# Performance work log

Measured on AMD Instinct MI355X. Metric: run time of the kernel, lower is better.

## Reference

```python
import jax, jax.numpy as jnp
import numpy as np

ALPHA = 0.2  # LeakyReLU negative slope
NEG_BIG = -9e15

def setup_inputs() -> dict:
    key = jax.random.key(0)
    k1, k2, k3, k4 = jax.random.split(key, 4)
    N, F_in, F_out = 8192, 512, 64
    inp = jax.random.normal(k1, (N, F_in), dtype=jnp.float32)
    adj = jax.random.randint(k2, (N, N), 0, 2, dtype=jnp.int32)
    W = jax.random.normal(k3, (F_in, F_out), dtype=jnp.float32) * (1.414 / np.sqrt(F_in + F_out))
    a = jax.random.normal(k4, (2 * F_out, 1), dtype=jnp.float32) * 0.1
    return {"input": inp, "adj": adj, "W": W, "a": a}

def reference(input, adj, W, a):
    # h: [N, F_out]
    h = input @ W
    F_out = h.shape[1]
    # Decompose a into a1 (source part) and a2 (target part):
    a1 = a[:F_out, 0]   # [F_out]
    a2 = a[F_out:, 0]   # [F_out]
    s1 = h @ a1         # [N]
    s2 = h @ a2         # [N]
    e = s1[:, None] + s2[None, :]                      # [N, N]
    e = jnp.where(e > 0, e, ALPHA * e)                 # LeakyReLU
    e = jnp.where(adj > 0, e, jnp.float32(NEG_BIG))    # mask non-edges
    attention = jax.nn.softmax(e, axis=1)              # [N, N]
    # dropout with p=0.0 / eval mode -> identity
    h_prime = attention @ h                            # [N, F_out]
    return h_prime
```

## Files before the change

### kernel.cpp

```cpp
#include <hip/hip_runtime.h>
#include <hip/hip_bf16.h>

constexpr int N    = 8192;
constexpr int FIN  = 512;
constexpr int FOUT = 64;
constexpr int NSPLIT = 8;
constexpr int JCHUNK = N / NSPLIT;
constexpr int NSLICE = 4;
constexpr int JS     = JCHUNK / NSLICE;
constexpr int LROW   = JS + 8;

typedef __attribute__((ext_vector_type(8))) short short8;
typedef __attribute__((ext_vector_type(4))) float f32x4;

union BF2U { unsigned int u; __hip_bfloat162 h; };

__global__ __launch_bounds__(256) void k1_proj(
    const float* __restrict__ input, const float* __restrict__ W,
    const float* __restrict__ a, __hip_bfloat16* __restrict__ hbT,
    float* __restrict__ E1, float* __restrict__ F1,
    float* __restrict__ E2, float* __restrict__ F2)
{
    __shared__ __hip_bfloat16 tile[8][64];
    const int tid  = threadIdx.x;
    const int col  = tid & 63;
    const int g    = tid >> 6;
    const int rbase = blockIdx.x * 8;

    float acc[2] = {0.f, 0.f};
    const float* in0 = input + (size_t)(rbase + g * 2) * FIN;

    for (int k = 0; k < FIN; k += 8) {
        float w[8];
        #pragma unroll
        for (int q = 0; q < 8; ++q) w[q] = W[(k + q) * FOUT + col];
        const float4 x0a = *(const float4*)(in0 + 0 * FIN + k);
        const float4 x0b = *(const float4*)(in0 + 0 * FIN + k + 4);
        const float4 x1a = *(const float4*)(in0 + 1 * FIN + k);
        const float4 x1b = *(const float4*)(in0 + 1 * FIN + k + 4);
        acc[0] = fmaf(x0a.w, w[3], fmaf(x0a.z, w[2], fmaf(x0a.y, w[1], fmaf(x0a.x, w[0], acc[0]))));
        acc[0] = fmaf(x0b.w, w[7], fmaf(x0b.z, w[6], fmaf(x0b.y, w[5], fmaf(x0b.x, w[4], acc[0]))));
        acc[1] = fmaf(x1a.w, w[3], fmaf(x1a.z, w[2], fmaf(x1a.y, w[1], fmaf(x1a.x, w[0], acc[1]))));
        acc[1] = fmaf(x1b.w, w[7], fmaf(x1b.z, w[6], fmaf(x1b.y, w[5], fmaf(x1b.x, w[4], acc[1]))));
    }

    const float a1c = a[col];
    const float a2c = a[FOUT + col];
    #pragma unroll
    for (int q = 0; q < 2; ++q) {
        float r1 = acc[q] * a1c;
        float r2 = acc[q] * a2c;
        #pragma unroll
        for (int off = 32; off >= 1; off >>= 1) {
            r1 += __shfl_xor(r1, off, 64);
            r2 += __shfl_xor(r2, off, 64);
        }
        if (col == 0) {
            const int i = rbase + g * 2 + q;
            E1[i] = __expf(r1);
            F1[i] = __expf(0.2f * r1);
            E2[i] = __expf(r2);
            F2[i] = __expf(0.2f * r2);
        }
        tile[g * 2 + q][col] = __float2bfloat16(acc[q]);
    }
    __syncthreads();

    if (tid < 128) {
        const int c = tid >> 1, part = tid & 1;
        unsigned short v[4];
        #pragma unroll
        for (int u = 0; u < 4; ++u) {
            __hip_bfloat16 hv = tile[part * 4 + u][c];
            v[u] = *reinterpret_cast<unsigned short*>(&hv);
        }
        *(ushort4*)((unsigned short*)hbT + (size_t)c * N + rbase + part * 4) =
            make_ushort4(v[0], v[1], v[2], v[3]);
    }
}

__global__ __launch_bounds__(256, 4) void k2_attn(
    const int* __restrict__ adj,
    const float* __restrict__ E1, const float* __restrict__ F1,
    const float* __restrict__ E2, const float* __restrict__ F2,
    const unsigned short* __restrict__ hbT,
    float* __restrict__ pAcc, float* __restrict__ pZ)
{
    __shared__ unsigned short Bl[64 * LROW];
    __shared__ unsigned int   Ml[64 * 9];
    __shared__ float          E2l[JS];
    __shared__ float          F2l[JS];

    const int r   = blockIdx.x;
    const int s   = blockIdx.y;
    const int tid = threadIdx.x;
    const int w     = tid >> 6;
    const int lane  = tid & 63;
    const int row16 = lane & 15;
    const int quad  = lane >> 4;

    const int iloc = w * 16 + row16;
    const int i    = r * 64 + iloc;
    const float E1i = E1[i];
    const float F1i = F1[i];

    short8 ones;
    #pragma unroll
    for (int q = 0; q < 8; ++q) ones[q] = (short)0x3F80;

    f32x4 acc0 = {0.f, 0.f, 0.f, 0.f};
    f32x4 acc1 = {0.f, 0.f, 0.f, 0.f};
    f32x4 acc2 = {0.f, 0.f, 0.f, 0.f};
    f32x4 acc3 = {0.f, 0.f, 0.f, 0.f};
    f32x4 accz = {0.f, 0.f, 0.f, 0.f};

    for (int sl = 0; sl < NSLICE; ++sl) {
        const int jbeg = s * JCHUNK + sl * JS;

        #pragma unroll
        for (int rr = 0; rr < 8; ++rr) {
            const int seg = rr * 256 + tid;
            const int f = seg >> 5, o = seg & 31;
            const short8 v = *(const short8*)((const short*)hbT + (size_t)f * N + jbeg + o * 8);
            *(short8*)(&Bl[f * LROW + o * 8]) = v;
        }
        {
            unsigned char* Mlb = (unsigned char*)Ml;
            #pragma unroll
            for (int it = 0; it < 16; ++it) {
                const int rloc = it * 4 + w;
                const int4 av = *(const int4*)(adj + (size_t)(r * 64 + rloc) * N + jbeg + lane * 4);
                unsigned int nib =
                    (av.x != 0 ? 1u : 0u) | (av.y != 0 ? 2u : 0u) |
                    (av.z != 0 ? 4u : 0u) | (av.w != 0 ? 8u : 0u);
                const unsigned int other = __shfl_xor(nib, 1, 64);
                if (!(lane & 1))
                    Mlb[rloc * 36 + (lane >> 1)] = (unsigned char)(nib | (other << 4));
            }
        }
        E2l[tid] = E2[jbeg + tid];
        F2l[tid] = F2[jbeg + tid];
        __syncthreads();

        #pragma unroll
        for (int it = 0; it < JS / 32; ++it) {
            const int jj = it * 32 + quad * 8;

            const unsigned int mword = Ml[iloc * 9 + it];
            const unsigned int mbyte = (mword >> (8 * quad)) & 0xffu;

            const float4 eA = *(const float4*)(&E2l[jj]);
            const float4 eB = *(const float4*)(&E2l[jj + 4]);
            const float4 fA = *(const float4*)(&F2l[jj]);
            const float4 fB = *(const float4*)(&F2l[jj + 4]);

            const short8 b0 = *(const short8*)(&Bl[(row16 +  0) * LROW + jj]);
            const short8 b1 = *(const short8*)(&Bl[(row16 + 16) * LROW + jj]);
            const short8 b2 = *(const short8*)(&Bl[(row16 + 32) * LROW + jj]);
            const short8 b3 = *(const short8*)(&Bl[(row16 + 48) * LROW + jj]);

            float e2v[8], f2v[8];
            e2v[0] = eA.x; e2v[1] = eA.y; e2v[2] = eA.z; e2v[3] = eA.w;
            e2v[4] = eB.x; e2v[5] = eB.y; e2v[6] = eB.z; e2v[7] = eB.w;
            f2v[0] = fA.x; f2v[1] = fA.y; f2v[2] = fA.z; f2v[3] = fA.w;
            f2v[4] = fB.x; f2v[5] = fB.y; f2v[6] = fB.z; f2v[7] = fB.w;

            float pv[8];
            #pragma unroll
            for (int j = 0; j < 8; ++j) {
                float p = fmaxf(E1i * e2v[j], F1i * f2v[j]);
                pv[j] = ((mbyte >> j) & 1u) ? p : 0.f;
            }

            short8 afrag;
            #pragma unroll
            for (int jp = 0; jp < 4; ++jp) {
                BF2U cv;
                cv.h = __float22bfloat162_rn(make_float2(pv[2 * jp], pv[2 * jp + 1]));
                afrag[2 * jp]     = (short)(cv.u & 0xffffu);
                afrag[2 * jp + 1] = (short)(cv.u >> 16);
            }

            acc0 = __builtin_amdgcn_mfma_f32_16x16x32_bf16(afrag, b0, acc0, 0, 0, 0);
            acc1 = __builtin_amdgcn_mfma_f32_16x16x32_bf16(afrag, b1, acc1, 0, 0, 0);
            acc2 = __builtin_amdgcn_mfma_f32_16x16x32_bf16(afrag, b2, acc2, 0, 0, 0);
            acc3 = __builtin_amdgcn_mfma_f32_16x16x32_bf16(afrag, b3, acc3, 0, 0, 0);
            accz = __builtin_amdgcn_mfma_f32_16x16x32_bf16(afrag, ones, accz, 0, 0, 0);
        }
        __syncthreads();
    }

    if (row16 == 0) {
        #pragma unroll
        for (int reg = 0; reg < 4; ++reg)
            pZ[(size_t)s * N + r * 64 + w * 16 + quad * 4 + reg] = accz[reg];
    }

    float* outp = pAcc + ((size_t)s * N + (size_t)r * 64 + w * 16) * FOUT;
    #pragma unroll
    for (int reg = 0; reg < 4; ++reg) {
        const int row = quad * 4 + reg;
        outp[row * FOUT + ( 0 + row16)] = acc0[reg];
        outp[row * FOUT + (16 + row16)] = acc1[reg];
        outp[row * FOUT + (32 + row16)] = acc2[reg];
        outp[row * FOUT + (48 + row16)] = acc3[reg];
    }
}

__global__ __launch_bounds__(256) void k3_combine(
    const float* __restrict__ pAcc, const float* __restrict__ pZ,
    float* __restrict__ out)
{
    const int idx = blockIdx.x * 256 + threadIdx.x;
    const int i = idx >> 6;
    float num = 0.f, den = 0.f;
    #pragma unroll
    for (int s = 0; s < NSPLIT; ++s) {
        num += pAcc[(size_t)s * N * FOUT + idx];
        den += pZ[(size_t)s * N + i];
    }
    out[idx] = num / den;
}

extern "C" void kernel_launch(void* const* d_in, const int* in_sizes, int n_in,
                              void* d_out, int out_size, void* d_ws, size_t ws_size,
                              hipStream_t stream)
{
    const float* input = (const float*)d_in[0];
    const int*   adj   = (const int*)d_in[1];
    const float* W     = (const float*)d_in[2];
    const float* a     = (const float*)d_in[3];
    float* out = (float*)d_out;

    char* ws = (char*)d_ws;
    __hip_bfloat16* hbT = (__hip_bfloat16*)ws;
    float* E1   = (float*)(ws + (size_t)FOUT * N * 2);
    float* F1   = E1 + N;
    float* E2   = F1 + N;
    float* F2   = E2 + N;
    float* pZ   = F2 + N;
    float* pAcc = pZ + (size_t)NSPLIT * N;

    k1_proj<<<N / 8, 256, 0, stream>>>(input, W, a, hbT, E1, F1, E2, F2);

    dim3 g2(N / 64, NSPLIT);
    k2_attn<<<g2, 256, 0, stream>>>(adj, E1, F1, E2, F2,
                                    (const unsigned short*)hbT, pAcc, pZ);

    k3_combine<<<(N * FOUT) / 256, 256, 0, stream>>>(pAcc, pZ, out);
}
```

Baseline: 439.6 us.

## Preload whole adjacency mask chunk and E2/F2 up front, halve slice width

The adjacency bitmask and the E2/F2 vectors for the whole 1024-column chunk are now loaded into shared memory once at block start, instead of being reloaded every slice. NSLICE doubles to 8, so each hbT slice is 128 columns wide and its shared-memory buffer shrinks. The aim is larger, more contiguous adj reads per row with more loads in flight, and less per-slice staging work. In exchange there are more slice iterations and barriers, and the preload phase is not overlapped with compute.

```diff
diff --git a/kernel.cpp b/kernel.cpp
--- a/kernel.cpp
+++ b/kernel.cpp
@@ -6,7 +6,7 @@
 constexpr int FOUT = 64;
 constexpr int NSPLIT = 8;
 constexpr int JCHUNK = N / NSPLIT;
-constexpr int NSLICE = 4;
+constexpr int NSLICE = 8;
 constexpr int JS     = JCHUNK / NSLICE;
 constexpr int LROW   = JS + 8;
 
@@ -87,9 +87,9 @@
     float* __restrict__ pAcc, float* __restrict__ pZ)
 {
     __shared__ unsigned short Bl[64 * LROW];
-    __shared__ unsigned int   Ml[64 * 9];
-    __shared__ float          E2l[JS];
-    __shared__ float          F2l[JS];
+    __shared__ unsigned int   Ml[64 * 33];
+    __shared__ float          E2l[JCHUNK];
+    __shared__ float          F2l[JCHUNK];
 
     const int r   = blockIdx.x;
     const int s   = blockIdx.y;
@@ -98,6 +98,31 @@
     const int lane  = tid & 63;
     const int row16 = lane & 15;
     const int quad  = lane >> 4;
+    const int jcbeg = s * JCHUNK;
+
+    *(float4*)(&E2l[tid * 4]) = *(const float4*)(E2 + jcbeg + tid * 4);
+    *(float4*)(&F2l[tid * 4]) = *(const float4*)(F2 + jcbeg + tid * 4);
+
+    {
+        unsigned char* Mlb = (unsigned char*)Ml;
+        #pragma unroll 4
+        for (int rr = 0; rr < 16; ++rr) {
+            const int rloc = w * 16 + rr;
+            const int* rowp = adj + (size_t)(r * 64 + rloc) * N + jcbeg;
+            #pragma unroll
+            for (int u = 0; u < 4; ++u) {
+                const int4 av = *(const int4*)(rowp + u * 256 + lane * 4);
+                unsigned int nib =
+                    (av.x != 0 ? 1u : 0u) | (av.y != 0 ? 2u : 0u) |
+                    (av.z != 0 ? 4u : 0u) | (av.w != 0 ? 8u : 0u);
+                const unsigned int other = __shfl_xor(nib, 1, 64);
+                if (!(lane & 1))
+                    Mlb[rloc * 132 + u * 32 + (lane >> 1)] =
+                        (unsigned char)(nib | (other << 4));
+            }
+        }
+    }
+    __syncthreads();
 
     const int iloc = w * 16 + row16;
     const int i    = r * 64 + iloc;
@@ -115,44 +140,28 @@
     f32x4 accz = {0.f, 0.f, 0.f, 0.f};
 
     for (int sl = 0; sl < NSLICE; ++sl) {
-        const int jbeg = s * JCHUNK + sl * JS;
-
-        #pragma unroll
-        for (int rr = 0; rr < 8; ++rr) {
+        #pragma unroll
+        for (int rr = 0; rr < 4; ++rr) {
             const int seg = rr * 256 + tid;
-            const int f = seg >> 5, o = seg & 31;
-            const short8 v = *(const short8*)((const short*)hbT + (size_t)f * N + jbeg + o * 8);
+            const int f = seg >> 4, o = seg & 15;
+            const short8 v = *(const short8*)((const short*)hbT +
+                               (size_t)f * N + jcbeg + sl * JS + o * 8);
             *(short8*)(&Bl[f * LROW + o * 8]) = v;
         }
-        {
-            unsigned char* Mlb = (unsigned char*)Ml;
-            #pragma unroll
-            for (int it = 0; it < 16; ++it) {
-                const int rloc = it * 4 + w;
-                const int4 av = *(const int4*)(adj + (size_t)(r * 64 + rloc) * N + jbeg + lane * 4);
-                unsigned int nib =
-                    (av.x != 0 ? 1u : 0u) | (av.y != 0 ? 2u : 0u) |
-                    (av.z != 0 ? 4u : 0u) | (av.w != 0 ? 8u : 0u);
-                const unsigned int other = __shfl_xor(nib, 1, 64);
-                if (!(lane & 1))
-                    Mlb[rloc * 36 + (lane >> 1)] = (unsigned char)(nib | (other << 4));
-            }
-        }
-        E2l[tid] = E2[jbeg + tid];
-        F2l[tid] = F2[jbeg + tid];
         __syncthreads();
 
         #pragma unroll
         for (int it = 0; it < JS / 32; ++it) {
-            const int jj = it * 32 + quad * 8;
-
-            const unsigned int mword = Ml[iloc * 9 + it];
+            const int jj  = it * 32 + quad * 8;
+            const int jja = sl * JS + jj;
+
+            const unsigned int mword = Ml[iloc * 33 + sl * 4 + it];
             const unsigned int mbyte = (mword >> (8 * quad)) & 0xffu;
 
-            const float4 eA = *(const float4*)(&E2l[jj]);
-            const float4 eB = *(const float4*)(&E2l[jj + 4]);
-            const float4 fA = *(const float4*)(&F2l[jj]);
-            const float4 fB = *(const float4*)(&F2l[jj + 4]);
+            const float4 eA = *(const float4*)(&E2l[jja]);
+            const float4 eB = *(const float4*)(&E2l[jja + 4]);
+            const float4 fA = *(const float4*)(&F2l[jja]);
+            const float4 fB = *(const float4*)(&F2l[jja + 4]);
 
             const short8 b0 = *(const short8*)(&Bl[(row16 +  0) * LROW + jj]);
             const short8 b1 = *(const short8*)(&Bl[(row16 + 16) * LROW + jj]);
```

Measured after the change: 457.7 us. 1.04x slower.

## Prefetch half of next adjacency slice into registers and rotate slice order

Applied to the files above, without the earlier changes.

Half of each wave's adjacency rows for the next slice are now loaded into registers before the compute loop runs, so those global loads overlap with the MFMA work instead of stalling at the slice start. The row-to-wave mapping changes so each wave handles 16 contiguous rows, and the slice order is rotated by the block row index to spread concurrent accesses across memory. The cost is 32 extra VGPRs for the prefetch buffer plus a fully unrolled slice loop, which could reduce occupancy.

```diff
diff --git a/kernel.cpp b/kernel.cpp
--- a/kernel.cpp
+++ b/kernel.cpp
@@ -114,8 +114,43 @@
     f32x4 acc3 = {0.f, 0.f, 0.f, 0.f};
     f32x4 accz = {0.f, 0.f, 0.f, 0.f};
 
-    for (int sl = 0; sl < NSLICE; ++sl) {
+    unsigned char* Mlb = (unsigned char*)Ml;
+
+    int4 pf[8];
+    {
+        const int jb0 = s * JCHUNK + ((0 + r) & (NSLICE - 1)) * JS;
+        #pragma unroll
+        for (int rr = 0; rr < 8; ++rr)
+            pf[rr] = *(const int4*)(adj + (size_t)(r * 64 + w * 16 + rr) * N + jb0 + lane * 4);
+    }
+
+    #pragma unroll
+    for (int slix = 0; slix < NSLICE; ++slix) {
+        const int sl   = (slix + r) & (NSLICE - 1);
         const int jbeg = s * JCHUNK + sl * JS;
+
+        #pragma unroll
+        for (int rr = 0; rr < 8; ++rr) {
+            const int rloc = w * 16 + rr;
+            const int4 av = pf[rr];
+            unsigned int nib =
+                (av.x != 0 ? 1u : 0u) | (av.y != 0 ? 2u : 0u) |
+                (av.z != 0 ? 4u : 0u) | (av.w != 0 ? 8u : 0u);
+            const unsigned int other = __shfl_xor(nib, 1, 64);
+            if (!(lane & 1))
+                Mlb[rloc * 36 + (lane >> 1)] = (unsigned char)(nib | (other << 4));
+        }
+        #pragma unroll
+        for (int rr = 8; rr < 16; ++rr) {
+            const int rloc = w * 16 + rr;
+            const int4 av = *(const int4*)(adj + (size_t)(r * 64 + rloc) * N + jbeg + lane * 4);
+            unsigned int nib =
+                (av.x != 0 ? 1u : 0u) | (av.y != 0 ? 2u : 0u) |
+                (av.z != 0 ? 4u : 0u) | (av.w != 0 ? 8u : 0u);
+            const unsigned int other = __shfl_xor(nib, 1, 64);
+            if (!(lane & 1))
+                Mlb[rloc * 36 + (lane >> 1)] = (unsigned char)(nib | (other << 4));
+        }
 
         #pragma unroll
         for (int rr = 0; rr < 8; ++rr) {
@@ -124,23 +159,16 @@
             const short8 v = *(const short8*)((const short*)hbT + (size_t)f * N + jbeg + o * 8);
             *(short8*)(&Bl[f * LROW + o * 8]) = v;
         }
-        {
-            unsigned char* Mlb = (unsigned char*)Ml;
-            #pragma unroll
-            for (int it = 0; it < 16; ++it) {
-                const int rloc = it * 4 + w;
-                const int4 av = *(const int4*)(adj + (size_t)(r * 64 + rloc) * N + jbeg + lane * 4);
-                unsigned int nib =
-                    (av.x != 0 ? 1u : 0u) | (av.y != 0 ? 2u : 0u) |
-                    (av.z != 0 ? 4u : 0u) | (av.w != 0 ? 8u : 0u);
-                const unsigned int other = __shfl_xor(nib, 1, 64);
-                if (!(lane & 1))
-                    Mlb[rloc * 36 + (lane >> 1)] = (unsigned char)(nib | (other << 4));
-            }
-        }
         E2l[tid] = E2[jbeg + tid];
         F2l[tid] = F2[jbeg + tid];
         __syncthreads();
+
+        if (slix + 1 < NSLICE) {
+            const int jbn = s * JCHUNK + (((slix + 1) + r) & (NSLICE - 1)) * JS;
+            #pragma unroll
+            for (int rr = 0; rr < 8; ++rr)
+                pf[rr] = *(const int4*)(adj + (size_t)(r * 64 + w * 16 + rr) * N + jbn + lane * 4);
+        }
 
         #pragma unroll
         for (int it = 0; it < JS / 32; ++it) {
```

Measured after the change: 462.4 us. 5.2% more time.
